# Optimization experiments

Hardware: AMD Instinct MI355X
Metric: run time of the kernel (lower is better)

The kernel has to match this reference:

```python
import jax, jax.numpy as jnp
import numpy as np

MODEL_DIM = 1024
NUM_HEADS = 16
K_DIM = MODEL_DIM // NUM_HEADS


def setup_inputs() -> dict:
    key = jax.random.key(0)
    kx, kw1, kw2 = jax.random.split(key, 3)
    B, L, D = 4, 2048, MODEL_DIM
    x = jax.random.normal(kx, (B, L, D), dtype=jnp.float32)
    # nn.Linear(D, 3D, bias=False): y = x @ W^T; store transposed form [D, 3D]
    scale1 = 1.0 / np.sqrt(D)
    Wqkv = jax.random.uniform(kw1, (D, 3 * D), dtype=jnp.float32, minval=-scale1, maxval=scale1)
    Wout = jax.random.uniform(kw2, (D, D), dtype=jnp.float32, minval=-scale1, maxval=scale1)
    return {"x": x, "Wqkv": Wqkv, "Wout": Wout}


def reference(x, Wqkv, Wout):
    B, L, D = x.shape
    H, Kd = NUM_HEADS, K_DIM
    qkv = x @ Wqkv  # [B, L, 3D]
    q, k, v = jnp.split(qkv, 3, axis=-1)

    def heads(t):  # [B, L, D] -> [B, H, L, Kd]
        return t.reshape(B, L, H, Kd).transpose(0, 2, 1, 3)

    qh, kh, vh = heads(q), heads(k), heads(v)
    scores = jnp.einsum('bhqd,bhkd->bhqk', qh, kh) / jnp.sqrt(jnp.float32(Kd))
    causal = jnp.triu(jnp.ones((L, L), dtype=bool), k=1)  # True above diagonal
    scores = jnp.where(causal, -jnp.inf, scores)
    probs = jax.nn.softmax(scores, axis=-1)
    attended = jnp.einsum('bhqk,bhkd->bhqd', probs, vh)
    concatted = attended.transpose(0, 2, 1, 3).reshape(B, L, D)
    # dropout is identity in eval mode
    return concatted @ Wout
```

## Files before the change

### kernel.cpp

```cpp
#include <hip/hip_runtime.h>

typedef unsigned short u16;
typedef unsigned int   u32;
typedef __bf16   bf16x8 __attribute__((ext_vector_type(8)));
typedef float    f32x4  __attribute__((ext_vector_type(4)));
typedef u16      u16x4  __attribute__((ext_vector_type(4)));
typedef u16      u16x8  __attribute__((ext_vector_type(8)));
typedef u32      u32x2  __attribute__((ext_vector_type(2)));
typedef u32      u32x4  __attribute__((ext_vector_type(4)));

#if __has_builtin(__builtin_amdgcn_exp2f)
#define EXP2(x) __builtin_amdgcn_exp2f(x)
#else
#define EXP2(x) exp2f(x)
#endif

__device__ __forceinline__ u16 f2bf(float f) {
    unsigned u = __float_as_uint(f);
    u += 0x7FFFu + ((u >> 16) & 1u);
    return (u16)(u >> 16);
}

__device__ __forceinline__ u32 pack_bf16(float a, float b) {
#if __has_builtin(__builtin_amdgcn_cvt_pk_bf16_f32)
    typedef __bf16 bf16x2 __attribute__((ext_vector_type(2)));
    bf16x2 r = __builtin_amdgcn_cvt_pk_bf16_f32(a, b);
    return __builtin_bit_cast(u32, r);
#else
    return (u32)f2bf(a) | ((u32)f2bf(b) << 16);
#endif
}

__device__ __forceinline__ void async_copy16(const u16* g, u16* l) {
    __builtin_amdgcn_global_load_lds(
        (const __attribute__((address_space(1))) unsigned*)g,
        (__attribute__((address_space(3))) unsigned*)l, 16, 0, 0);
}

__device__ __forceinline__ bf16x8 lds_frag(const u16* p) {
    return *(const bf16x8*)p;
}

__device__ __forceinline__ void permlane32_swap(u32& a, u32& b) {
    asm("v_permlane32_swap_b32 %0, %1" : "+v"(a), "+v"(b));
}
__device__ __forceinline__ void permlane16_swap(u32& a, u32& b) {
    asm("v_permlane16_swap_b32 %0, %1" : "+v"(a), "+v"(b));
}

__global__ __launch_bounds__(256) void prep(const float* __restrict__ x,
                                            const float* __restrict__ Wqkv,
                                            const float* __restrict__ Wout,
                                            u16* __restrict__ xb,
                                            u16* __restrict__ wqkv_t,
                                            u16* __restrict__ wout_t) {
    __shared__ u16 t[64 * 72];
    const int bid = blockIdx.x;
    const int tid = threadIdx.x;

    if (bid >= 1024) {
        size_t i = ((size_t)(bid - 1024) * 256 + tid) * 8;
        float4 v0 = *(const float4*)(x + i);
        float4 v1 = *(const float4*)(x + i + 4);
        u16x8 o = { f2bf(v0.x), f2bf(v0.y), f2bf(v0.z), f2bf(v0.w),
                    f2bf(v1.x), f2bf(v1.y), f2bf(v1.z), f2bf(v1.w) };
        *(u16x8*)(xb + i) = o;
        return;
    }

    const float* W;  u16* Wt;  int Kd, Nd, n0, k0;
    if (bid < 768) { W = Wqkv; Wt = wqkv_t; Kd = 1024; Nd = 3072;
                     n0 = (bid % 48) * 64; k0 = (bid / 48) * 64; }
    else           { W = Wout; Wt = wout_t; Kd = 1024; Nd = 1024;
                     n0 = ((bid - 768) % 16) * 64; k0 = ((bid - 768) / 16) * 64; }
#pragma unroll
    for (int i = 0; i < 4; ++i) {
        int lin = i * 256 + tid;
        int kr = lin >> 4, nc = (lin & 15) << 2;
        float4 v = *(const float4*)(W + (size_t)(k0 + kr) * Nd + n0 + nc);
        u16x4 o = { f2bf(v.x), f2bf(v.y), f2bf(v.z), f2bf(v.w) };
        *(u16x4*)&t[kr * 72 + nc] = o;
    }
    __syncthreads();
#pragma unroll
    for (int i = 0; i < 2; ++i) {
        int lin = i * 256 + tid;
        int nr = lin >> 3, kc = (lin & 7) << 3;
        u16x8 o;
#pragma unroll
        for (int jj = 0; jj < 8; ++jj) o[jj] = t[(kc + jj) * 72 + nr];
        *(u16x8*)(Wt + (size_t)(n0 + nr) * Kd + k0 + kc) = o;
    }
}

__global__ __launch_bounds__(256) void gemm_qkv(const u16* __restrict__ A,
                                                const u16* __restrict__ Bt,
                                                u16* __restrict__ outb,
                                                int K, int N) {
    __shared__ u16 As[2][128 * 32];
    __shared__ u16 Bs[2][128 * 32];
    const int tid = threadIdx.x;
    const int lane = tid & 63;
    const int wv = tid >> 6;
    const int wr = (wv >> 1) * 64;
    const int wc = (wv & 1) * 64;
    const int qd = lane >> 4;
    const int c  = lane & 15;
    const int m0 = blockIdx.y * 128;
    const int n0 = blockIdx.x * 128;

    const int srow = tid >> 2;
    const int sg = ((tid & 3) ^ ((srow >> 1) & 3)) << 3;

    const u16* Ag0 = A  + (size_t)(m0 +      srow) * K + sg;
    const u16* Ag1 = A  + (size_t)(m0 + 64 + srow) * K + sg;
    const u16* Bg0 = Bt + (size_t)(n0 +      srow) * K + sg;
    const u16* Bg1 = Bt + (size_t)(n0 + 64 + srow) * K + sg;

    const u32 fsw = (qd ^ ((c >> 1) & 3)) << 3;
    const u32 a_off = (wr + c) * 32 + fsw;
    const u32 b_off = (wc + c) * 32 + fsw;

    f32x4 acc[4][4] = {};

    async_copy16(Ag0, &As[0][tid * 8]);
    async_copy16(Ag1, &As[0][2048 + tid * 8]);
    async_copy16(Bg0, &Bs[0][tid * 8]);
    async_copy16(Bg1, &Bs[0][2048 + tid * 8]);

    int p = 0;
    for (int k0 = 0; k0 < K; k0 += 32) {
        __syncthreads();
        if (k0 + 32 < K) {
            const int np = p ^ 1;
            async_copy16(Ag0 + k0 + 32, &As[np][tid * 8]);
            async_copy16(Ag1 + k0 + 32, &As[np][2048 + tid * 8]);
            async_copy16(Bg0 + k0 + 32, &Bs[np][tid * 8]);
            async_copy16(Bg1 + k0 + 32, &Bs[np][2048 + tid * 8]);
        }
        bf16x8 af[4], bfr[4];
#pragma unroll
        for (int i = 0; i < 4; ++i) af[i]  = lds_frag(&As[p][a_off + i * 512]);
#pragma unroll
        for (int j = 0; j < 4; ++j) bfr[j] = lds_frag(&Bs[p][b_off + j * 512]);
#pragma unroll
        for (int i = 0; i < 4; ++i)
#pragma unroll
            for (int j = 0; j < 4; ++j)
                acc[i][j] = __builtin_amdgcn_mfma_f32_16x16x32_bf16(af[i], bfr[j], acc[i][j], 0, 0, 0);
        p ^= 1;
    }

#pragma unroll
    for (int i = 0; i < 4; ++i)
#pragma unroll
        for (int j = 0; j < 4; ++j) {
            int n = n0 + wc + j * 16 + c;
            int which = n >> 10, h = (n >> 6) & 15, kd = n & 63;
            int m_base = m0 + wr + i * 16 + qd * 4;
            int b = m_base >> 11, l0 = m_base & 2047;
            int bh = b * 16 + h;
            if (which == 2) {
                u32x2 o2;
                o2[0] = pack_bf16(acc[i][j][0], acc[i][j][1]);
                o2[1] = pack_bf16(acc[i][j][2], acc[i][j][3]);
                *(u32x2*)(outb + (size_t)(128 + bh) * 131072 + (size_t)kd * 2048 + l0) = o2;
            } else if (which == 0) {
#pragma unroll
                for (int r = 0; r < 4; ++r)
                    outb[(size_t)bh * 131072 + (size_t)(l0 + r) * 64 + kd] =
                        f2bf(acc[i][j][r] * 0.1803368801f);
            } else {
#pragma unroll
                for (int r = 0; r < 4; ++r)
                    outb[(size_t)(64 + bh) * 131072 + (size_t)(l0 + r) * 64 + kd] =
                        f2bf(acc[i][j][r]);
            }
        }
}

__global__ __launch_bounds__(256) void gemm_out(const u16* __restrict__ A,
                                                const u16* __restrict__ Bt,
                                                float* __restrict__ outf,
                                                int K, int N) {
    __shared__ u16 As[2][64 * 32];
    __shared__ u16 Bs[2][128 * 32];
    const int tid = threadIdx.x;
    const int lane = tid & 63;
    const int wv = tid >> 6;
    const int wr = (wv >> 1) * 32;
    const int wc = (wv & 1) * 64;
    const int qd = lane >> 4;
    const int c  = lane & 15;
    const int m0 = blockIdx.y * 64;
    const int n0 = blockIdx.x * 128;

    const int srow = tid >> 2;
    const int sg = ((tid & 3) ^ ((srow >> 1) & 3)) << 3;

    const u16* Ag0 = A  + (size_t)(m0 +      srow) * K + sg;
    const u16* Bg0 = Bt + (size_t)(n0 +      srow) * K + sg;
    const u16* Bg1 = Bt + (size_t)(n0 + 64 + srow) * K + sg;

    const u32 fsw = (qd ^ ((c >> 1) & 3)) << 3;
    const u32 a_off = (wr + c) * 32 + fsw;
    const u32 b_off = (wc + c) * 32 + fsw;

    f32x4 acc[2][4] = {};

    async_copy16(Ag0, &As[0][tid * 8]);
    async_copy16(Bg0, &Bs[0][tid * 8]);
    async_copy16(Bg1, &Bs[0][2048 + tid * 8]);

    int p = 0;
    for (int k0 = 0; k0 < K; k0 += 32) {
        __syncthreads();
        if (k0 + 32 < K) {
            const int np = p ^ 1;
            async_copy16(Ag0 + k0 + 32, &As[np][tid * 8]);
            async_copy16(Bg0 + k0 + 32, &Bs[np][tid * 8]);
            async_copy16(Bg1 + k0 + 32, &Bs[np][2048 + tid * 8]);
        }
        bf16x8 af[2], bfr[4];
#pragma unroll
        for (int i = 0; i < 2; ++i) af[i]  = lds_frag(&As[p][a_off + i * 512]);
#pragma unroll
        for (int j = 0; j < 4; ++j) bfr[j] = lds_frag(&Bs[p][b_off + j * 512]);
#pragma unroll
        for (int i = 0; i < 2; ++i)
#pragma unroll
            for (int j = 0; j < 4; ++j)
                acc[i][j] = __builtin_amdgcn_mfma_f32_16x16x32_bf16(af[i], bfr[j], acc[i][j], 0, 0, 0);
        p ^= 1;
    }

#pragma unroll
    for (int i = 0; i < 2; ++i)
#pragma unroll
        for (int j = 0; j < 4; ++j)
#pragma unroll
            for (int r = 0; r < 4; ++r) {
                int m = m0 + wr + i * 16 + qd * 4 + r;
                int n = n0 + wc + j * 16 + c;
                outf[(size_t)m * N + n] = acc[i][j][r];
            }
}

__global__ __launch_bounds__(256, 2) void attn_kernel(const u16* __restrict__ qkv,
                                                      u16* __restrict__ att) {
    __shared__ u16 Ks[2][128 * 64];
    __shared__ u16 Vt[3][64 * 128];

    const int tid = threadIdx.x;
    const int lane = tid & 63;
    const int w = tid >> 6;
    const int qd = lane >> 4;
    const int c = lane & 15;

    const int flat = blockIdx.x + 8 * blockIdx.y;
    const int bh = (flat & 7) + 8 * ((flat >> 3) & 7);
    const int bx = flat >> 6;
    const int b = bh >> 4, h = bh & 15;

    const u16* Qg = qkv + (size_t)bh * 131072;
    const u16* Kg = qkv + (size_t)(64 + bh) * 131072;
    const u16* Vg = qkv + (size_t)(128 + bh) * 131072;

    u32 kf_off[2];
#pragma unroll
    for (int ks = 0; ks < 2; ++ks)
        kf_off[ks] = c * 64 + (((ks * 4 + qd) ^ (c & 7)) << 3);
    u32 vf_off[4];
#pragma unroll
    for (int kc = 0; kc < 4; ++kc)
        vf_off[kc] = c * 128 + (((kc * 4 + qd) ^ c) << 3);

    auto issue_copy = [&](int t, u16* kd, u16* vd) {
#pragma unroll
        for (int it = 0; it < 4; ++it) {
            int lin = it * 256 + tid;
            int krw = lin >> 3, kch = lin & 7;
            int vrw = lin >> 4, vch = lin & 15;
            async_copy16(Kg + (size_t)t * 8192 + krw * 64 + ((kch ^ (krw & 7)) << 3),
                         kd + lin * 8);
            async_copy16(Vg + (size_t)t * 128 + (size_t)vrw * 2048 + ((vch ^ (vrw & 15)) << 3),
                         vd + lin * 8);
        }
    };

#pragma unroll 1
    for (int seg = 0; seg < 2; ++seg) {
        const int qt = seg ? (15 - bx) : bx;
        const int qa_row = qt * 128 + w * 32 + c;
        const int qb_row = qa_row + 16;

        bf16x8 qa[2], qb[2];
#pragma unroll
        for (int ks = 0; ks < 2; ++ks) {
            qa[ks] = *(const bf16x8*)(Qg + (size_t)qa_row * 64 + ks * 32 + qd * 8);
            qb[ks] = *(const bf16x8*)(Qg + (size_t)qb_row * 64 + ks * 32 + qd * 8);
        }

        f32x4 acca[4] = {}, accb[4] = {};
        f32x4 rva = {}, rvb = {};
        f32x4 saA[8], sbA[8], saB[8], sbB[8];

        const int nkt = qt + 1;

        auto compute_S = [&](const u16* ksb, f32x4* sa, f32x4* sb) {
#pragma unroll
            for (int f = 0; f < 8; ++f) {
                sa[f] = f32x4{-8.f, -8.f, -8.f, -8.f};
                sb[f] = f32x4{-8.f, -8.f, -8.f, -8.f};
            }
            __builtin_amdgcn_s_setprio(1);
#pragma unroll
            for (int ks = 0; ks < 2; ++ks) {
                const u16* kp = ksb + kf_off[ks];
#pragma unroll
                for (int f = 0; f < 8; ++f) {
                    bf16x8 kf = lds_frag(kp + f * 1024);
                    sa[f] = __builtin_amdgcn_mfma_f32_16x16x32_bf16(kf, qa[ks], sa[f], 0, 0, 0);
                    sb[f] = __builtin_amdgcn_mfma_f32_16x16x32_bf16(kf, qb[ks], sb[f], 0, 0, 0);
                }
            }
            __builtin_amdgcn_s_setprio(0);
        };

        auto finish_tile = [&](int kt, f32x4* sa, f32x4* sb, const u16* vtb) {
            if (kt == qt) {
#pragma unroll
                for (int f = 0; f < 8; ++f)
#pragma unroll
                    for (int r = 0; r < 4; ++r) {
                        int key = kt * 128 + f * 16 + qd * 4 + r;
                        if (key > qa_row) sa[f][r] = -3e38f;
                        if (key > qb_row) sb[f][r] = -3e38f;
                    }
            }
#pragma unroll
            for (int f = 0; f < 8; ++f) {
#pragma unroll
                for (int r = 0; r < 4; ++r) {
                    sa[f][r] = EXP2(sa[f][r]);
                    sb[f][r] = EXP2(sb[f][r]);
                }
                rva += sa[f];
                rvb += sb[f];
            }
#pragma unroll
            for (int kc = 0; kc < 4; ++kc) {
                u32 a0 = pack_bf16(sa[2 * kc][0], sa[2 * kc][1]);
                u32 a1 = pack_bf16(sa[2 * kc + 1][0], sa[2 * kc + 1][1]);
                u32 b0 = pack_bf16(sa[2 * kc][2], sa[2 * kc][3]);
                u32 b1 = pack_bf16(sa[2 * kc + 1][2], sa[2 * kc + 1][3]);
                permlane32_swap(a0, a1); permlane16_swap(a0, a1);
                permlane32_swap(b0, b1); permlane16_swap(b0, b1);
                u32x4 wa = {a0, b0, a1, b1};
                u32 c0 = pack_bf16(sb[2 * kc][0], sb[2 * kc][1]);
                u32 c1 = pack_bf16(sb[2 * kc + 1][0], sb[2 * kc + 1][1]);
                u32 d0 = pack_bf16(sb[2 * kc][2], sb[2 * kc][3]);
                u32 d1 = pack_bf16(sb[2 * kc + 1][2], sb[2 * kc + 1][3]);
                permlane32_swap(c0, c1); permlane16_swap(c0, c1);
                permlane32_swap(d0, d1); permlane16_swap(d0, d1);
                u32x4 wb = {c0, d0, c1, d1};
                bf16x8 pa = __builtin_bit_cast(bf16x8, wa);
                bf16x8 pb = __builtin_bit_cast(bf16x8, wb);
                const u16* vp = vtb + vf_off[kc];
                __builtin_amdgcn_s_setprio(1);
#pragma unroll
                for (int jo = 0; jo < 4; ++jo) {
                    bf16x8 vf = lds_frag(vp + jo * 2048);
                    acca[jo] = __builtin_amdgcn_mfma_f32_16x16x32_bf16(vf, pa, acca[jo], 0, 0, 0);
                    accb[jo] = __builtin_amdgcn_mfma_f32_16x16x32_bf16(vf, pb, accb[jo], 0, 0, 0);
                }
                __builtin_amdgcn_s_setprio(0);
            }
        };

        __syncthreads();
        issue_copy(0, Ks[0], Vt[0]);
        __syncthreads();
        if (nkt > 1) issue_copy(1, Ks[1], Vt[1]);
        compute_S(Ks[0], saA, sbA);

        u16 *vPV = Vt[0], *vNx = Vt[1], *vFr = Vt[2];

        int kt = 0;
        for (;;) {
            {
                const bool last = (kt + 1 >= nkt);
                if (!last) {
                    __syncthreads();
                    if (kt + 2 < nkt) issue_copy(kt + 2, Ks[0], vFr);
                    compute_S(Ks[1], saB, sbB);
                }
                finish_tile(kt, saA, sbA, vPV);
                if (last) break;
                u16* t0 = vPV; vPV = vNx; vNx = vFr; vFr = t0;
            }
            {
                const bool last = (kt + 2 >= nkt);
                if (!last) {
                    __syncthreads();
                    if (kt + 3 < nkt) issue_copy(kt + 3, Ks[1], vFr);
                    compute_S(Ks[0], saA, sbA);
                }
                finish_tile(kt + 1, saB, sbB, vPV);
                if (last) break;
                u16* t0 = vPV; vPV = vNx; vNx = vFr; vFr = t0;
            }
            kt += 2;
        }

        float ra = rva[0] + rva[1] + rva[2] + rva[3];
        float rb = rvb[0] + rvb[1] + rvb[2] + rvb[3];
        ra += __shfl_xor(ra, 16, 64);
        ra += __shfl_xor(ra, 32, 64);
        rb += __shfl_xor(rb, 16, 64);
        rb += __shfl_xor(rb, 32, 64);
        float ia = __builtin_amdgcn_rcpf(ra), ib = __builtin_amdgcn_rcpf(rb);
        u16* ar = att + ((size_t)b * 2048 + qa_row) * 1024 + h * 64;
        u16* br = att + ((size_t)b * 2048 + qb_row) * 1024 + h * 64;
#pragma unroll
        for (int jo = 0; jo < 4; ++jo) {
            u32x2 oa, ob;
            oa[0] = pack_bf16(acca[jo][0] * ia, acca[jo][1] * ia);
            oa[1] = pack_bf16(acca[jo][2] * ia, acca[jo][3] * ia);
            ob[0] = pack_bf16(accb[jo][0] * ib, accb[jo][1] * ib);
            ob[1] = pack_bf16(accb[jo][2] * ib, accb[jo][3] * ib);
            *(u32x2*)(ar + jo * 16 + qd * 4) = oa;
            *(u32x2*)(br + jo * 16 + qd * 4) = ob;
        }
    }
}

extern "C" void kernel_launch(void* const* d_in, const int* in_sizes, int n_in,
                              void* d_out, int out_size, void* d_ws, size_t ws_size,
                              hipStream_t stream) {
    const float* x    = (const float*)d_in[0];
    const float* Wqkv = (const float*)d_in[1];
    const float* Wout = (const float*)d_in[2];
    float* out = (float*)d_out;

    char* ws = (char*)d_ws;
    u16* x_bf   = (u16*)(ws);
    u16* wqkv_t = (u16*)(ws + 16777216);
    u16* wout_t = (u16*)(ws + 23068672);
    u16* qkv_h  = (u16*)(ws + 25165824);
    u16* att    = (u16*)(ws + 75497472);

    prep<<<dim3(5120), dim3(256), 0, stream>>>(x, Wqkv, Wout, x_bf, wqkv_t, wout_t);
    gemm_qkv<<<dim3(24, 64), dim3(256), 0, stream>>>(x_bf, wqkv_t, qkv_h, 1024, 3072);
    attn_kernel<<<dim3(8, 64), dim3(256), 0, stream>>>(qkv_h, att);
    gemm_out<<<dim3(8, 128), dim3(256), 0, stream>>>(att, wout_t, out, 1024, 1024);
}
```

Baseline: 270.2 us.

## Interleave per-half-tile S computation with softmax/PV to halve live score registers

```diff
diff --git a/kernel.cpp b/kernel.cpp
--- a/kernel.cpp
+++ b/kernel.cpp
@@ -246,6 +246,56 @@
             }
 }
 
+#define ATTN_COMPUTE_S(KSB, QARR, S)                                          \
+    do {                                                                      \
+        _Pragma("unroll") for (int f = 0; f < 8; ++f)                         \
+            S[f] = f32x4{-8.f, -8.f, -8.f, -8.f};                             \
+        __builtin_amdgcn_s_setprio(1);                                        \
+        _Pragma("unroll") for (int ks = 0; ks < 2; ++ks) {                    \
+            const u16* kp = (KSB) + kf_off[ks];                               \
+            _Pragma("unroll") for (int f = 0; f < 8; ++f) {                   \
+                bf16x8 kf = lds_frag(kp + f * 1024);                          \
+                S[f] = __builtin_amdgcn_mfma_f32_16x16x32_bf16(               \
+                    kf, QARR[ks], S[f], 0, 0, 0);                             \
+            }                                                                 \
+        }                                                                     \
+        __builtin_amdgcn_s_setprio(0);                                        \
+    } while (0)
+
+#define ATTN_FINISH(S, QROW, RV, ACC, VTB, KT)                                \
+    do {                                                                      \
+        if ((KT) == qt) {                                                     \
+            _Pragma("unroll") for (int f = 0; f < 8; ++f)                     \
+                _Pragma("unroll") for (int r = 0; r < 4; ++r) {               \
+                    int key = (KT) * 128 + f * 16 + qd * 4 + r;               \
+                    if (key > (QROW)) S[f][r] = -3e38f;                       \
+                }                                                             \
+        }                                                                     \
+        _Pragma("unroll") for (int f = 0; f < 8; ++f) {                       \
+            _Pragma("unroll") for (int r = 0; r < 4; ++r)                     \
+                S[f][r] = EXP2(S[f][r]);                                      \
+            RV += S[f];                                                       \
+        }                                                                     \
+        _Pragma("unroll") for (int kc = 0; kc < 4; ++kc) {                    \
+            u32 a0 = pack_bf16(S[2 * kc][0], S[2 * kc][1]);                   \
+            u32 a1 = pack_bf16(S[2 * kc + 1][0], S[2 * kc + 1][1]);           \
+            u32 b0 = pack_bf16(S[2 * kc][2], S[2 * kc][3]);                   \
+            u32 b1 = pack_bf16(S[2 * kc + 1][2], S[2 * kc + 1][3]);           \
+            permlane32_swap(a0, a1); permlane16_swap(a0, a1);                 \
+            permlane32_swap(b0, b1); permlane16_swap(b0, b1);                 \
+            u32x4 wpk = {a0, b0, a1, b1};                                     \
+            bf16x8 pfrag = __builtin_bit_cast(bf16x8, wpk);                   \
+            const u16* vp = (VTB) + vf_off[kc];                               \
+            __builtin_amdgcn_s_setprio(1);                                    \
+            _Pragma("unroll") for (int jo = 0; jo < 4; ++jo) {                \
+                bf16x8 vf = lds_frag(vp + jo * 2048);                         \
+                ACC[jo] = __builtin_amdgcn_mfma_f32_16x16x32_bf16(            \
+                    vf, pfrag, ACC[jo], 0, 0, 0);                             \
+            }                                                                 \
+            __builtin_amdgcn_s_setprio(0);                                    \
+        }                                                                     \
+    } while (0)
+
 __global__ __launch_bounds__(256, 2) void attn_kernel(const u16* __restrict__ qkv,
                                                       u16* __restrict__ att) {
     __shared__ u16 Ks[2][128 * 64];
@@ -303,114 +353,29 @@
 
         f32x4 acca[4] = {}, accb[4] = {};
         f32x4 rva = {}, rvb = {};
-        f32x4 saA[8], sbA[8], saB[8], sbB[8];
+        f32x4 sa[8], sb[8];
 
         const int nkt = qt + 1;
-
-        auto compute_S = [&](const u16* ksb, f32x4* sa, f32x4* sb) {
-#pragma unroll
-            for (int f = 0; f < 8; ++f) {
-                sa[f] = f32x4{-8.f, -8.f, -8.f, -8.f};
-                sb[f] = f32x4{-8.f, -8.f, -8.f, -8.f};
-            }
-            __builtin_amdgcn_s_setprio(1);
-#pragma unroll
-            for (int ks = 0; ks < 2; ++ks) {
-                const u16* kp = ksb + kf_off[ks];
-#pragma unroll
-                for (int f = 0; f < 8; ++f) {
-                    bf16x8 kf = lds_frag(kp + f * 1024);
-                    sa[f] = __builtin_amdgcn_mfma_f32_16x16x32_bf16(kf, qa[ks], sa[f], 0, 0, 0);
-                    sb[f] = __builtin_amdgcn_mfma_f32_16x16x32_bf16(kf, qb[ks], sb[f], 0, 0, 0);
-                }
-            }
-            __builtin_amdgcn_s_setprio(0);
-        };
-
-        auto finish_tile = [&](int kt, f32x4* sa, f32x4* sb, const u16* vtb) {
-            if (kt == qt) {
-#pragma unroll
-                for (int f = 0; f < 8; ++f)
-#pragma unroll
-                    for (int r = 0; r < 4; ++r) {
-                        int key = kt * 128 + f * 16 + qd * 4 + r;
-                        if (key > qa_row) sa[f][r] = -3e38f;
-                        if (key > qb_row) sb[f][r] = -3e38f;
-                    }
-            }
-#pragma unroll
-            for (int f = 0; f < 8; ++f) {
-#pragma unroll
-                for (int r = 0; r < 4; ++r) {
-                    sa[f][r] = EXP2(sa[f][r]);
-                    sb[f][r] = EXP2(sb[f][r]);
-                }
-                rva += sa[f];
-                rvb += sb[f];
-            }
-#pragma unroll
-            for (int kc = 0; kc < 4; ++kc) {
-                u32 a0 = pack_bf16(sa[2 * kc][0], sa[2 * kc][1]);
-                u32 a1 = pack_bf16(sa[2 * kc + 1][0], sa[2 * kc + 1][1]);
-                u32 b0 = pack_bf16(sa[2 * kc][2], sa[2 * kc][3]);
-                u32 b1 = pack_bf16(sa[2 * kc + 1][2], sa[2 * kc + 1][3]);
-                permlane32_swap(a0, a1); permlane16_swap(a0, a1);
-                permlane32_swap(b0, b1); permlane16_swap(b0, b1);
-                u32x4 wa = {a0, b0, a1, b1};
-                u32 c0 = pack_bf16(sb[2 * kc][0], sb[2 * kc][1]);
-                u32 c1 = pack_bf16(sb[2 * kc + 1][0], sb[2 * kc + 1][1]);
-                u32 d0 = pack_bf16(sb[2 * kc][2], sb[2 * kc][3]);
-                u32 d1 = pack_bf16(sb[2 * kc + 1][2], sb[2 * kc + 1][3]);
-                permlane32_swap(c0, c1); permlane16_swap(c0, c1);
-                permlane32_swap(d0, d1); permlane16_swap(d0, d1);
-                u32x4 wb = {c0, d0, c1, d1};
-                bf16x8 pa = __builtin_bit_cast(bf16x8, wa);
-                bf16x8 pb = __builtin_bit_cast(bf16x8, wb);
-                const u16* vp = vtb + vf_off[kc];
-                __builtin_amdgcn_s_setprio(1);
-#pragma unroll
-                for (int jo = 0; jo < 4; ++jo) {
-                    bf16x8 vf = lds_frag(vp + jo * 2048);
-                    acca[jo] = __builtin_amdgcn_mfma_f32_16x16x32_bf16(vf, pa, acca[jo], 0, 0, 0);
-                    accb[jo] = __builtin_amdgcn_mfma_f32_16x16x32_bf16(vf, pb, accb[jo], 0, 0, 0);
-                }
-                __builtin_amdgcn_s_setprio(0);
-            }
-        };
 
         __syncthreads();
         issue_copy(0, Ks[0], Vt[0]);
         __syncthreads();
         if (nkt > 1) issue_copy(1, Ks[1], Vt[1]);
-        compute_S(Ks[0], saA, sbA);
+        ATTN_COMPUTE_S(Ks[0], qa, sa);
 
         u16 *vPV = Vt[0], *vNx = Vt[1], *vFr = Vt[2];
 
-        int kt = 0;
-        for (;;) {
-            {
-                const bool last = (kt + 1 >= nkt);
-                if (!last) {
-                    __syncthreads();
-                    if (kt + 2 < nkt) issue_copy(kt + 2, Ks[0], vFr);
-                    compute_S(Ks[1], saB, sbB);
-                }
-                finish_tile(kt, saA, sbA, vPV);
-                if (last) break;
-                u16* t0 = vPV; vPV = vNx; vNx = vFr; vFr = t0;
+#pragma unroll 1
+        for (int kt = 0; kt < nkt; ++kt) {
+            ATTN_COMPUTE_S(Ks[kt & 1], qb, sb);
+            ATTN_FINISH(sa, qa_row, rva, acca, vPV, kt);
+            if (kt + 1 < nkt) {
+                __syncthreads();
+                if (kt + 2 < nkt) issue_copy(kt + 2, Ks[kt & 1], vFr);
+                ATTN_COMPUTE_S(Ks[(kt + 1) & 1], qa, sa);
             }
-            {
-                const bool last = (kt + 2 >= nkt);
-                if (!last) {
-                    __syncthreads();
-                    if (kt + 3 < nkt) issue_copy(kt + 3, Ks[1], vFr);
-                    compute_S(Ks[0], saA, sbA);
-                }
-                finish_tile(kt + 1, saB, sbB, vPV);
-                if (last) break;
-                u16* t0 = vPV; vPV = vNx; vNx = vFr; vFr = t0;
-            }
-            kt += 2;
+            ATTN_FINISH(sb, qb_row, rvb, accb, vPV, kt);
+            u16* t0 = vPV; vPV = vNx; vNx = vFr; vFr = t0;
         }
 
         float ra = rva[0] + rva[1] + rva[2] + rva[3];
```

Result: faster. 250.3 us (-7.4%).
